# Kernel tuning notes

Hardware: AMD Instinct MI355X
Metric: run time of the kernel (lower is better)

Reference implementation:

```python
import jax, jax.numpy as jnp
import numpy as np

BETA = 0.25
K = 1024   # num_codebook_vectors
D = 256    # latent_dim


def setup_inputs() -> dict:
    key = jax.random.key(0)
    k1, k2 = jax.random.split(key)
    z = jax.random.normal(k1, (16, D, 64, 64), dtype=jnp.float32)
    # embedding initialized uniform(-1/K, 1/K) as in the torch module
    emb = jax.random.uniform(k2, (K, D), dtype=jnp.float32, minval=-1.0 / K, maxval=1.0 / K)
    return {"z": z, "emb": emb}


def reference(z, emb):
    sg = jax.lax.stop_gradient
    # NCHW -> NHWC
    z_nhwc = jnp.transpose(z, (0, 2, 3, 1))            # [B,H,W,D]
    zf = z_nhwc.reshape(-1, D)                          # [N,D]
    # squared euclidean distances: ||z||^2 + ||e||^2 - 2 z e^T
    d = (jnp.sum(zf * zf, axis=1, keepdims=True)
         + jnp.sum(emb * emb, axis=1)
         - 2.0 * jnp.matmul(zf, emb.T))                 # [N,K]
    min_encoding_indices = jnp.argmin(d, axis=1)        # [N] int
    z_q = emb[min_encoding_indices].reshape(z_nhwc.shape)  # [B,H,W,D]
    # loss exactly as in source (first term is zero in value, faithful)
    loss = (jnp.mean((sg(z_nhwc) - z_nhwc) ** 2)
            + BETA * jnp.mean((z_q - sg(z_nhwc)) ** 2))
    # straight-through estimator
    z_q_st = z_nhwc + sg(z_q - z_nhwc)
    out = jnp.transpose(z_q_st, (0, 3, 1, 2))           # NHWC -> NCHW
    return out, min_encoding_indices, loss
```

## Files before the change

kernel.cpp:

```cpp
#include <hip/hip_runtime.h>

#define DD 256
#define KK 1024
#define HW 4096
#define NROWSZ 65536
#define OUT_Z 16777216
#define OUT_IDX OUT_Z
#define OUT_LOSS (OUT_Z + NROWSZ)

#define MARGIN 4.5e-4f

#define WS_ESQ   0
#define WS_EH    4096
#define WS_HLIST 528384
#define WS_HCNT  790528
#define WS_LSUM  790536
#define WS_EMBT  791552
#define WS_EHP   1840128

typedef _Float16 f16x8 __attribute__((ext_vector_type(8)));
typedef float f32x4 __attribute__((ext_vector_type(4)));
union U16x8 { uint4 u; f16x8 h; };
typedef unsigned long long u64;

static __device__ __forceinline__ u64 umin64(u64 a, u64 b) { return a < b ? a : b; }
static __device__ __forceinline__ unsigned pk16(float a, float b) {
    _Float16 ha = (_Float16)a, hb = (_Float16)b;
    return (unsigned)__builtin_bit_cast(unsigned short, ha)
         | ((unsigned)__builtin_bit_cast(unsigned short, hb) << 16);
}

__global__ void vq_prep(const float* __restrict__ emb, float* __restrict__ esq,
                        uint2* __restrict__ eh2, int* __restrict__ hcnt,
                        double* __restrict__ lsum, float* __restrict__ embT,
                        int use_embT, uint4* __restrict__ ehP, int use_ehp)
{
    const int bid = blockIdx.x;
    const int t = threadIdx.x;
    if (bid == 0 && t == 0) { *hcnt = 0; *lsum = 0.0; }

    if (bid < 4) {
        int k = bid * 256 + t;
        const float* e = emb + (size_t)k * DD;
        float blk[2];
#pragma unroll
        for (int b2 = 0; b2 < 2; ++b2) {
            const float* p = e + b2 * 128;
            float r[8];
#pragma unroll
            for (int j = 0; j < 8; ++j) r[j] = __fmul_rn(p[j], p[j]);
            for (int i = 8; i < 128; i += 8) {
#pragma unroll
                for (int j = 0; j < 8; ++j)
                    r[j] = __fadd_rn(r[j], __fmul_rn(p[i + j], p[i + j]));
            }
            blk[b2] = __fadd_rn(__fadd_rn(__fadd_rn(r[0], r[1]), __fadd_rn(r[2], r[3])),
                                __fadd_rn(__fadd_rn(r[4], r[5]), __fadd_rn(r[6], r[7])));
        }
        esq[k] = __fadd_rn(blk[0], blk[1]);
    } else if (bid < 20) {
        int tid = (bid - 4) * 256 + t;
        const float4* e4 = (const float4*)emb;
#pragma unroll
        for (int i = 0; i < 16; ++i) {
            int idx = i * 4096 + tid;
            float4 v = e4[idx];
            eh2[idx] = make_uint2(pk16(v.x, v.y), pk16(v.z, v.w));
        }
    } else if (bid < 36) {
        if (!use_embT) return;
        int u = bid - 20;
        int k = u * 64 + (t >> 2);
        int c = t & 3;
        const float4* e4 = (const float4*)(emb + (size_t)k * DD);
#pragma unroll
        for (int i = 0; i < 16; ++i) {
            float4 v = e4[c * 16 + i];
            int d = c * 64 + i * 4;
            embT[(size_t)(d + 0) * KK + k] = v.x;
            embT[(size_t)(d + 1) * KK + k] = v.y;
            embT[(size_t)(d + 2) * KK + k] = v.z;
            embT[(size_t)(d + 3) * KK + k] = v.w;
        }
    } else {
        if (!use_ehp) return;
#pragma unroll
        for (int it = 0; it < 8; ++it) {
            int L = ((bid - 36) * 8 + it) * 256 + t;
            int lane = L & 63, ds = (L >> 6) & 7, t16 = L >> 9;
            int col = lane & 15, quad = lane >> 4;
            int code = t16 * 16 + col;
            int d0 = ds * 32 + quad * 8;
            const float* e = emb + (size_t)code * DD + d0;
            float4 a = *(const float4*)e;
            float4 c4 = *(const float4*)(e + 4);
            ehP[L] = make_uint4(pk16(a.x, a.y), pk16(a.z, a.w),
                                pk16(c4.x, c4.y), pk16(c4.z, c4.w));
        }
    }
}

__launch_bounds__(512, 2)
__global__ void vq_score(const float* __restrict__ z, const _Float16* __restrict__ eh,
                         const uint4* __restrict__ ehP, const float* __restrict__ esq,
                         float* __restrict__ out, int* __restrict__ hlist,
                         int* __restrict__ hcnt, int use_ehp)
{
    __shared__ __align__(16) char zh[256 * 512];
    __shared__ float esq_s[1024];
    __shared__ uint2 cand[256];

    const int t = threadIdx.x;
    const int lane = t & 63;
    const int w = t >> 6;
    const int col = lane & 15;
    const int quad = lane >> 4;

    const int n0 = blockIdx.x * 256;
    const int b = n0 >> 12;
    const int hw0 = n0 & (HW - 1);

    {
        const int row = t & 255;
        const int dh = t >> 8;
        const float* src = z + (size_t)b * DD * HW + hw0 + row;
#pragma unroll
        for (int i = 0; i < 16; ++i) {
            const int d0 = dh * 128 + i * 8;
            float v0 = src[(size_t)(d0 + 0) * HW];
            float v1 = src[(size_t)(d0 + 1) * HW];
            float v2 = src[(size_t)(d0 + 2) * HW];
            float v3 = src[(size_t)(d0 + 3) * HW];
            float v4 = src[(size_t)(d0 + 4) * HW];
            float v5 = src[(size_t)(d0 + 5) * HW];
            float v6 = src[(size_t)(d0 + 6) * HW];
            float v7 = src[(size_t)(d0 + 7) * HW];
            uint4 pk = make_uint4(pk16(v0, v1), pk16(v2, v3), pk16(v4, v5), pk16(v6, v7));
            *(uint4*)(zh + (size_t)row * 512 + ((d0 * 2) ^ ((row & 7) << 4))) = pk;
        }
        esq_s[t] = esq[t];
        esq_s[512 + t] = esq[512 + t];
    }
    __syncthreads();

    U16x8 af[2][8];
#pragma unroll
    for (int nt = 0; nt < 2; ++nt) {
        const int row = w * 32 + nt * 16 + col;
        const int sw = (row & 7) << 4;
#pragma unroll
        for (int ds = 0; ds < 8; ++ds)
            af[nt][ds].u = *(const uint4*)(zh + (size_t)row * 512
                                           + ((ds * 64 + quad * 16) ^ sw));
    }

    unsigned t1[8], t2[8];
#pragma unroll
    for (int i = 0; i < 8; ++i) { t1[i] = 0xFFFFFFFFu; t2[i] = 0xFFFFFFFFu; }

    auto proc = [&](U16x8 (&bf)[8], int t16) {
        const int code = t16 * 16 + col;
        const float eq1 = 1.0f + esq_s[code];
        f32x4 acc0 = (f32x4)0.0f, acc1 = (f32x4)0.0f;
#pragma unroll
        for (int ds = 0; ds < 8; ++ds) {
            acc0 = __builtin_amdgcn_mfma_f32_16x16x32_f16(af[0][ds].h, bf[ds].h, acc0, 0, 0, 0);
            acc1 = __builtin_amdgcn_mfma_f32_16x16x32_f16(af[1][ds].h, bf[ds].h, acc1, 0, 0, 0);
        }
#pragma unroll
        for (int r = 0; r < 4; ++r) {
            float s0 = fmaf(-2.0f, acc0[r], eq1);
            unsigned k0 = (__float_as_uint(s0) & 0xFFFFFC00u) | (unsigned)code;
            t2[r] = min(t2[r], max(t1[r], k0));
            t1[r] = min(t1[r], k0);
            float s1 = fmaf(-2.0f, acc1[r], eq1);
            unsigned k1 = (__float_as_uint(s1) & 0xFFFFFC00u) | (unsigned)code;
            t2[4 + r] = min(t2[4 + r], max(t1[4 + r], k1));
            t1[4 + r] = min(t1[4 + r], k1);
        }
    };

    if (use_ehp) {
        const uint4* bq = ehP + lane;
        U16x8 bfA[8], bfB[8];
#pragma unroll
        for (int ds = 0; ds < 8; ++ds) bfA[ds].u = bq[ds * 64];
#pragma unroll 1
        for (int t16 = 0; t16 < 64; t16 += 2) {
            const uint4* p1 = bq + (size_t)(t16 + 1) * 512;
#pragma unroll
            for (int ds = 0; ds < 8; ++ds) bfB[ds].u = p1[ds * 64];
            proc(bfA, t16);
            const uint4* p2 = bq + (size_t)((t16 + 2) & 63) * 512;
#pragma unroll
            for (int ds = 0; ds < 8; ++ds) bfA[ds].u = p2[ds * 64];
            proc(bfB, t16 + 1);
            if ((t16 & 6) == 6) __builtin_amdgcn_s_barrier();
        }
    } else {
        const uint4* ehq = (const uint4*)eh;
#pragma unroll 1
        for (int t16 = 0; t16 < 64; ++t16) {
            const uint4* bp = ehq + (size_t)(t16 * 16 + col) * 32 + quad;
            U16x8 bf[8];
#pragma unroll
            for (int ds = 0; ds < 8; ++ds) bf[ds].u = bp[ds * 4];
            proc(bf, t16);
        }
    }

#pragma unroll
    for (int mi = 0; mi < 8; ++mi) {
        unsigned a = t1[mi], bb = t2[mi];
#pragma unroll
        for (int off = 1; off < 16; off <<= 1) {
            unsigned o1 = __shfl_xor(a, off, 16);
            unsigned o2 = __shfl_xor(bb, off, 16);
            unsigned mx = max(a, o1);
            a = min(a, o1);
            bb = min(min(bb, o2), mx);
        }
        if (col == 0)
            cand[w * 32 + (mi >> 2) * 16 + quad * 4 + (mi & 3)] = make_uint2(a, bb);
    }
    __syncthreads();

    if (t < 256) {
        uint2 c = cand[t];
        float s1 = __uint_as_float(c.x & 0xFFFFFC00u);
        float s2 = __uint_as_float(c.y & 0xFFFFFC00u);
        int k1 = (int)(c.x & 1023u);
        if (__fsub_rn(s2, s1) > MARGIN) {
            out[OUT_IDX + n0 + t] = (float)k1;
        } else {
            int pos = atomicAdd(hcnt, 1);
            hlist[pos] = n0 + t;
        }
    }
}

template<int USET>
static __device__ __forceinline__ void dot_codes(const float4* __restrict__ embT4,
                                                 const float4* __restrict__ emb4,
                                                 const float4* __restrict__ zb4,
                                                 int t, float (&acc_)[8][4])
{
#pragma unroll 2
    for (int dc = 0; dc < 64; ++dc) {
        float4 e0, e1, e2, e3;
        if (USET) {
            e0 = embT4[(size_t)(dc * 4 + 0) * 256 + t];
            e1 = embT4[(size_t)(dc * 4 + 1) * 256 + t];
            e2 = embT4[(size_t)(dc * 4 + 2) * 256 + t];
            e3 = embT4[(size_t)(dc * 4 + 3) * 256 + t];
        } else {
            float4 a0 = emb4[(size_t)(4 * t + 0) * 64 + dc];
            float4 a1 = emb4[(size_t)(4 * t + 1) * 64 + dc];
            float4 a2 = emb4[(size_t)(4 * t + 2) * 64 + dc];
            float4 a3 = emb4[(size_t)(4 * t + 3) * 64 + dc];
            e0 = make_float4(a0.x, a1.x, a2.x, a3.x);
            e1 = make_float4(a0.y, a1.y, a2.y, a3.y);
            e2 = make_float4(a0.z, a1.z, a2.z, a3.z);
            e3 = make_float4(a0.w, a1.w, a2.w, a3.w);
        }
#pragma unroll
        for (int j = 0; j < 8; ++j) {
            float4 zv = zb4[j * 64 + dc];
            acc_[j][0] = fmaf(zv.x, e0.x, acc_[j][0]);
            acc_[j][1] = fmaf(zv.x, e0.y, acc_[j][1]);
            acc_[j][2] = fmaf(zv.x, e0.z, acc_[j][2]);
            acc_[j][3] = fmaf(zv.x, e0.w, acc_[j][3]);
            acc_[j][0] = fmaf(zv.y, e1.x, acc_[j][0]);
            acc_[j][1] = fmaf(zv.y, e1.y, acc_[j][1]);
            acc_[j][2] = fmaf(zv.y, e1.z, acc_[j][2]);
            acc_[j][3] = fmaf(zv.y, e1.w, acc_[j][3]);
            acc_[j][0] = fmaf(zv.z, e2.x, acc_[j][0]);
            acc_[j][1] = fmaf(zv.z, e2.y, acc_[j][1]);
            acc_[j][2] = fmaf(zv.z, e2.z, acc_[j][2]);
            acc_[j][3] = fmaf(zv.z, e2.w, acc_[j][3]);
            acc_[j][0] = fmaf(zv.w, e3.x, acc_[j][0]);
            acc_[j][1] = fmaf(zv.w, e3.y, acc_[j][1]);
            acc_[j][2] = fmaf(zv.w, e3.z, acc_[j][2]);
            acc_[j][3] = fmaf(zv.w, e3.w, acc_[j][3]);
        }
    }
}

__launch_bounds__(256)
__global__ void vq_hard(const float* __restrict__ z, const float* __restrict__ emb,
                        const float* __restrict__ embT, const float* __restrict__ esq,
                        const int* __restrict__ hlist, const int* __restrict__ hcnt,
                        float* __restrict__ out, int use_embT)
{
    __shared__ __align__(16) float zbuf[8 * 256];
    __shared__ float chains[8][16];
    __shared__ float zq_s[8];
    __shared__ int rows_s[8];
    __shared__ u64 red[4][8];

    const int t = threadIdx.x;
    const int lane = t & 63;
    const int w = t >> 6;
    const int count = *hcnt;

    const float4* embT4 = (const float4*)embT;
    const float4* emb4 = (const float4*)emb;
    const float4* zb4 = (const float4*)zbuf;
    const float4 eqv4 = ((const float4*)esq)[t];
    const float eqa[4] = {eqv4.x, eqv4.y, eqv4.z, eqv4.w};

    for (int g = blockIdx.x; g * 8 < count; g += gridDim.x) {
        __syncthreads();
        if (t < 8) {
            int p = g * 8 + t;
            rows_s[t] = (p < count) ? hlist[p] : -1;
        }
        __syncthreads();

        {
            const int j = t >> 5, dpos = t & 31;
            const int r = rows_s[j];
            float4 v0 = make_float4(0.f, 0.f, 0.f, 0.f), v1 = v0;
            if (r >= 0) {
                const float* zp = z + (size_t)(r >> 12) * (DD * HW) + (r & (HW - 1));
                const int d0 = dpos * 8;
                v0.x = zp[(size_t)(d0 + 0) * HW];
                v0.y = zp[(size_t)(d0 + 1) * HW];
                v0.z = zp[(size_t)(d0 + 2) * HW];
                v0.w = zp[(size_t)(d0 + 3) * HW];
                v1.x = zp[(size_t)(d0 + 4) * HW];
                v1.y = zp[(size_t)(d0 + 5) * HW];
                v1.z = zp[(size_t)(d0 + 6) * HW];
                v1.w = zp[(size_t)(d0 + 7) * HW];
            }
            *(float4*)&zbuf[j * 256 + dpos * 8] = v0;
            *(float4*)&zbuf[j * 256 + dpos * 8 + 4] = v1;
        }
        __syncthreads();

        if (t < 128) {
            int j = t >> 4, c = t & 15, b2 = c >> 3, jj = c & 7;
            const float* p = &zbuf[j * 256];
            int base = b2 * 128 + jj;
            float v = p[base];
            float acc = __fmul_rn(v, v);
            for (int i = 1; i < 16; ++i) {
                float u = p[base + i * 8];
                acc = __fadd_rn(acc, __fmul_rn(u, u));
            }
            chains[j][c] = acc;
        }
        __syncthreads();
        if (t < 8) {
            const float* c = chains[t];
            float b0 = __fadd_rn(__fadd_rn(__fadd_rn(c[0], c[1]), __fadd_rn(c[2], c[3])),
                                 __fadd_rn(__fadd_rn(c[4], c[5]), __fadd_rn(c[6], c[7])));
            float b1 = __fadd_rn(__fadd_rn(__fadd_rn(c[8], c[9]), __fadd_rn(c[10], c[11])),
                                 __fadd_rn(__fadd_rn(c[12], c[13]), __fadd_rn(c[14], c[15])));
            zq_s[t] = __fadd_rn(b0, b1);
        }
        __syncthreads();

        float acc_[8][4];
#pragma unroll
        for (int j = 0; j < 8; ++j)
#pragma unroll
            for (int kk = 0; kk < 4; ++kk) acc_[j][kk] = 0.0f;

        if (use_embT) dot_codes<1>(embT4, emb4, zb4, t, acc_);
        else          dot_codes<0>(embT4, emb4, zb4, t, acc_);

#pragma unroll
        for (int j = 0; j < 8; ++j) {
            u64 m = ~0ull;
#pragma unroll
            for (int kk = 0; kk < 4; ++kk) {
                float s = __fsub_rn(__fadd_rn(zq_s[j], eqa[kk]),
                                    __fmul_rn(2.0f, acc_[j][kk]));
                u64 p = ((u64)__float_as_uint(s) << 32) | (unsigned)(4 * t + kk);
                m = umin64(m, p);
            }
#pragma unroll
            for (int off = 1; off < 64; off <<= 1)
                m = umin64(m, __shfl_xor(m, off, 64));
            if (lane == 0) red[w][j] = m;
        }
        __syncthreads();
        if (t < 8) {
            u64 m = umin64(umin64(red[0][t], red[1][t]), umin64(red[2][t], red[3][t]));
            int r = rows_s[t];
            if (r >= 0) out[OUT_IDX + r] = (float)(int)(m & 0xffffffffu);
        }
    }
}

__launch_bounds__(256)
__global__ void vq_out(const float* __restrict__ z, const float* __restrict__ emb,
                       const float* __restrict__ embT, float* out,
                       double* __restrict__ lsum, int use_embT)
{
    __shared__ float et[8 * 1024];
    __shared__ float wsum[4];

    const int t = threadIdx.x;
    const int lane = t & 63;
    const int w = t >> 6;
    const int bb = blockIdx.x >> 5;
    const int dg = blockIdx.x & 31;

    if (use_embT) {
#pragma unroll
        for (int c = 0; c < 8; ++c)
            *(float4*)&et[c * 1024 + t * 4] =
                *(const float4*)&embT[(size_t)(dg * 8 + c) * KK + t * 4];
    } else {
        for (int i = 0; i < 32; ++i) {
            int kk = i * 256 + t;
            et[kk] = emb[(size_t)(kk & 1023) * DD + dg * 8 + (kk >> 10)];
        }
    }
    __syncthreads();

    float lacc = 0.f;
    const size_t zb = (size_t)bb * DD * HW;
    const float* idxf = out + OUT_IDX + (size_t)bb * HW;
#pragma unroll
    for (int ch = 0; ch < 4; ++ch) {
        const int hw = ch * 1024 + t * 4;
        float4 fi = *(const float4*)&idxf[hw];
        int k0 = (int)fi.x, k1 = (int)fi.y, k2 = (int)fi.z, k3 = (int)fi.w;
#pragma unroll
        for (int dl = 0; dl < 8; ++dl) {
            size_t off = zb + (size_t)(dg * 8 + dl) * HW + hw;
            float4 zv = *(const float4*)&z[off];
            float4 e;
            e.x = et[dl * 1024 + k0];
            e.y = et[dl * 1024 + k1];
            e.z = et[dl * 1024 + k2];
            e.w = et[dl * 1024 + k3];
            *(float4*)&out[off] = e;
            float df;
            df = e.x - zv.x; lacc = fmaf(df, df, lacc);
            df = e.y - zv.y; lacc = fmaf(df, df, lacc);
            df = e.z - zv.z; lacc = fmaf(df, df, lacc);
            df = e.w - zv.w; lacc = fmaf(df, df, lacc);
        }
    }
#pragma unroll
    for (int off = 32; off > 0; off >>= 1) lacc += __shfl_down(lacc, off, 64);
    if (lane == 0) wsum[w] = lacc;
    __syncthreads();
    if (t == 0) {
        double tot = (double)wsum[0] + (double)wsum[1] + (double)wsum[2] + (double)wsum[3];
        atomicAdd(lsum, tot);
    }
}

__global__ void vq_final(const double* __restrict__ lsum, float* __restrict__ out)
{
    out[OUT_LOSS] = (float)(0.25 * (lsum[0] / (double)OUT_Z));
}

extern "C" void kernel_launch(void* const* d_in, const int* in_sizes, int n_in,
                              void* d_out, int out_size, void* d_ws, size_t ws_size,
                              hipStream_t stream)
{
    const float* z = (const float*)d_in[0];
    const float* emb = (const float*)d_in[1];
    float* out = (float*)d_out;
    char* w = (char*)d_ws;

    float* esq = (float*)(w + WS_ESQ);
    _Float16* eh = (_Float16*)(w + WS_EH);
    uint2* eh2 = (uint2*)(w + WS_EH);
    int* hlist = (int*)(w + WS_HLIST);
    int* hcnt = (int*)(w + WS_HCNT);
    double* lsum = (double*)(w + WS_LSUM);
    float* embT = (float*)(w + WS_EMBT);
    uint4* ehP = (uint4*)(w + WS_EHP);

    int use_embT = (ws_size >= (size_t)WS_EMBT + (size_t)DD * KK * sizeof(float)) ? 1 : 0;
    int use_ehp = (ws_size >= (size_t)WS_EHP + (size_t)KK * DD * sizeof(_Float16)) ? 1 : 0;

    vq_prep<<<dim3(52), dim3(256), 0, stream>>>(emb, esq, eh2, hcnt, lsum, embT, use_embT,
                                                ehP, use_ehp);
    vq_score<<<dim3(256), dim3(512), 0, stream>>>(z, eh, ehP, esq, out, hlist, hcnt,
                                                  use_ehp);
    vq_hard<<<dim3(1024), dim3(256), 0, stream>>>(z, emb, embT, esq, hlist, hcnt, out,
                                                  use_embT);
    vq_out<<<dim3(512), dim3(256), 0, stream>>>(z, emb, embT, out, lsum, use_embT);
    vq_final<<<dim3(1), dim3(1), 0, stream>>>(lsum, out);
}
```

Baseline: 247.4 us.

## Shrink vq_score and vq_out tiles to launch more blocks across CUs

vq_score now handles 64 rows per 256-thread block instead of 256 rows per 512-thread block. Each wave computes one 16-row MFMA tile instead of two, and the double-buffered codebook prefetch and periodic barrier are dropped. vq_out now covers 4 latent channels per block instead of 8, which doubles its grid. The aim is to fill all 256 CUs of the MI355X with more, smaller blocks. The cost is that each codebook fragment loaded from global memory now feeds only one MFMA tile, and without software prefetch there is less latency hiding.

```diff
diff --git a/kernel.cpp b/kernel.cpp
--- a/kernel.cpp
+++ b/kernel.cpp
@@ -100,15 +100,15 @@
     }
 }
 
-__launch_bounds__(512, 2)
+__launch_bounds__(256, 4)
 __global__ void vq_score(const float* __restrict__ z, const _Float16* __restrict__ eh,
                          const uint4* __restrict__ ehP, const float* __restrict__ esq,
                          float* __restrict__ out, int* __restrict__ hlist,
                          int* __restrict__ hcnt, int use_ehp)
 {
-    __shared__ __align__(16) char zh[256 * 512];
+    __shared__ __align__(16) char zh[64 * 512];
     __shared__ float esq_s[1024];
-    __shared__ uint2 cand[256];
+    __shared__ uint2 cand[64];
 
     const int t = threadIdx.x;
     const int lane = t & 63;
@@ -116,17 +116,15 @@
     const int col = lane & 15;
     const int quad = lane >> 4;
 
-    const int n0 = blockIdx.x * 256;
+    const int n0 = blockIdx.x * 64;
     const int b = n0 >> 12;
     const int hw0 = n0 & (HW - 1);
 
     {
-        const int row = t & 255;
-        const int dh = t >> 8;
-        const float* src = z + (size_t)b * DD * HW + hw0 + row;
-#pragma unroll
-        for (int i = 0; i < 16; ++i) {
-            const int d0 = dh * 128 + i * 8;
+        const float* src = z + (size_t)b * DD * HW + hw0 + lane;
+#pragma unroll
+        for (int i = 0; i < 8; ++i) {
+            const int d0 = w * 64 + i * 8;
             float v0 = src[(size_t)(d0 + 0) * HW];
             float v1 = src[(size_t)(d0 + 1) * HW];
             float v2 = src[(size_t)(d0 + 2) * HW];
@@ -136,81 +134,77 @@
             float v6 = src[(size_t)(d0 + 6) * HW];
             float v7 = src[(size_t)(d0 + 7) * HW];
             uint4 pk = make_uint4(pk16(v0, v1), pk16(v2, v3), pk16(v4, v5), pk16(v6, v7));
-            *(uint4*)(zh + (size_t)row * 512 + ((d0 * 2) ^ ((row & 7) << 4))) = pk;
+            *(uint4*)(zh + (size_t)lane * 512 + ((d0 * 2) ^ ((lane & 7) << 4))) = pk;
         }
         esq_s[t] = esq[t];
+        esq_s[256 + t] = esq[256 + t];
         esq_s[512 + t] = esq[512 + t];
+        esq_s[768 + t] = esq[768 + t];
     }
     __syncthreads();
 
-    U16x8 af[2][8];
-#pragma unroll
-    for (int nt = 0; nt < 2; ++nt) {
-        const int row = w * 32 + nt * 16 + col;
-        const int sw = (row & 7) << 4;
+    U16x8 af[8];
+    {
+        const int arow = w * 16 + col;
+        const int sw = (arow & 7) << 4;
 #pragma unroll
         for (int ds = 0; ds < 8; ++ds)
-            af[nt][ds].u = *(const uint4*)(zh + (size_t)row * 512
-                                           + ((ds * 64 + quad * 16) ^ sw));
-    }
-
-    unsigned t1[8], t2[8];
-#pragma unroll
-    for (int i = 0; i < 8; ++i) { t1[i] = 0xFFFFFFFFu; t2[i] = 0xFFFFFFFFu; }
-
-    auto proc = [&](U16x8 (&bf)[8], int t16) {
-        const int code = t16 * 16 + col;
-        const float eq1 = 1.0f + esq_s[code];
-        f32x4 acc0 = (f32x4)0.0f, acc1 = (f32x4)0.0f;
-#pragma unroll
-        for (int ds = 0; ds < 8; ++ds) {
-            acc0 = __builtin_amdgcn_mfma_f32_16x16x32_f16(af[0][ds].h, bf[ds].h, acc0, 0, 0, 0);
-            acc1 = __builtin_amdgcn_mfma_f32_16x16x32_f16(af[1][ds].h, bf[ds].h, acc1, 0, 0, 0);
-        }
-#pragma unroll
-        for (int r = 0; r < 4; ++r) {
-            float s0 = fmaf(-2.0f, acc0[r], eq1);
-            unsigned k0 = (__float_as_uint(s0) & 0xFFFFFC00u) | (unsigned)code;
-            t2[r] = min(t2[r], max(t1[r], k0));
-            t1[r] = min(t1[r], k0);
-            float s1 = fmaf(-2.0f, acc1[r], eq1);
-            unsigned k1 = (__float_as_uint(s1) & 0xFFFFFC00u) | (unsigned)code;
-            t2[4 + r] = min(t2[4 + r], max(t1[4 + r], k1));
-            t1[4 + r] = min(t1[4 + r], k1);
-        }
-    };
+            af[ds].u = *(const uint4*)(zh + (size_t)arow * 512
+                                       + ((ds * 64 + quad * 16) ^ sw));
+    }
+
+    unsigned t1[4], t2[4];
+#pragma unroll
+    for (int i = 0; i < 4; ++i) { t1[i] = 0xFFFFFFFFu; t2[i] = 0xFFFFFFFFu; }
 
     if (use_ehp) {
         const uint4* bq = ehP + lane;
-        U16x8 bfA[8], bfB[8];
-#pragma unroll
-        for (int ds = 0; ds < 8; ++ds) bfA[ds].u = bq[ds * 64];
 #pragma unroll 1
-        for (int t16 = 0; t16 < 64; t16 += 2) {
-            const uint4* p1 = bq + (size_t)(t16 + 1) * 512;
-#pragma unroll
-            for (int ds = 0; ds < 8; ++ds) bfB[ds].u = p1[ds * 64];
-            proc(bfA, t16);
-            const uint4* p2 = bq + (size_t)((t16 + 2) & 63) * 512;
-#pragma unroll
-            for (int ds = 0; ds < 8; ++ds) bfA[ds].u = p2[ds * 64];
-            proc(bfB, t16 + 1);
-            if ((t16 & 6) == 6) __builtin_amdgcn_s_barrier();
+        for (int t16 = 0; t16 < 64; ++t16) {
+            const uint4* p = bq + (size_t)t16 * 512;
+            U16x8 bf[8];
+#pragma unroll
+            for (int ds = 0; ds < 8; ++ds) bf[ds].u = p[ds * 64];
+            const int code = t16 * 16 + col;
+            const float eq1 = 1.0f + esq_s[code];
+            f32x4 acc = (f32x4)0.0f;
+#pragma unroll
+            for (int ds = 0; ds < 8; ++ds)
+                acc = __builtin_amdgcn_mfma_f32_16x16x32_f16(af[ds].h, bf[ds].h, acc, 0, 0, 0);
+#pragma unroll
+            for (int r = 0; r < 4; ++r) {
+                float s = fmaf(-2.0f, acc[r], eq1);
+                unsigned k = (__float_as_uint(s) & 0xFFFFFC00u) | (unsigned)code;
+                t2[r] = min(t2[r], max(t1[r], k));
+                t1[r] = min(t1[r], k);
+            }
         }
     } else {
         const uint4* ehq = (const uint4*)eh;
 #pragma unroll 1
         for (int t16 = 0; t16 < 64; ++t16) {
-            const uint4* bp = ehq + (size_t)(t16 * 16 + col) * 32 + quad;
+            const int code = t16 * 16 + col;
+            const uint4* bp = ehq + (size_t)code * 32 + quad;
             U16x8 bf[8];
 #pragma unroll
             for (int ds = 0; ds < 8; ++ds) bf[ds].u = bp[ds * 4];
-            proc(bf, t16);
-        }
-    }
-
-#pragma unroll
-    for (int mi = 0; mi < 8; ++mi) {
+            const float eq1 = 1.0f + esq_s[code];
+            f32x4 acc = (f32x4)0.0f;
+#pragma unroll
+            for (int ds = 0; ds < 8; ++ds)
+                acc = __builtin_amdgcn_mfma_f32_16x16x32_f16(af[ds].h, bf[ds].h, acc, 0, 0, 0);
+#pragma unroll
+            for (int r = 0; r < 4; ++r) {
+                float s = fmaf(-2.0f, acc[r], eq1);
+                unsigned k = (__float_as_uint(s) & 0xFFFFFC00u) | (unsigned)code;
+                t2[r] = min(t2[r], max(t1[r], k));
+                t1[r] = min(t1[r], k);
+            }
+        }
+    }
+
+#pragma unroll
+    for (int mi = 0; mi < 4; ++mi) {
         unsigned a = t1[mi], bb = t2[mi];
 #pragma unroll
         for (int off = 1; off < 16; off <<= 1) {
@@ -221,11 +215,11 @@
             bb = min(min(bb, o2), mx);
         }
         if (col == 0)
-            cand[w * 32 + (mi >> 2) * 16 + quad * 4 + (mi & 3)] = make_uint2(a, bb);
+            cand[w * 16 + quad * 4 + mi] = make_uint2(a, bb);
     }
     __syncthreads();
 
-    if (t < 256) {
+    if (t < 64) {
         uint2 c = cand[t];
         float s1 = __uint_as_float(c.x & 0xFFFFFC00u);
         float s2 = __uint_as_float(c.y & 0xFFFFFC00u);
@@ -399,24 +393,24 @@
                        const float* __restrict__ embT, float* out,
                        double* __restrict__ lsum, int use_embT)
 {
-    __shared__ float et[8 * 1024];
+    __shared__ float et[4 * 1024];
     __shared__ float wsum[4];
 
     const int t = threadIdx.x;
     const int lane = t & 63;
     const int w = t >> 6;
-    const int bb = blockIdx.x >> 5;
-    const int dg = blockIdx.x & 31;
+    const int bb = blockIdx.x >> 6;
+    const int dg = blockIdx.x & 63;
 
     if (use_embT) {
 #pragma unroll
-        for (int c = 0; c < 8; ++c)
+        for (int c = 0; c < 4; ++c)
             *(float4*)&et[c * 1024 + t * 4] =
-                *(const float4*)&embT[(size_t)(dg * 8 + c) * KK + t * 4];
+                *(const float4*)&embT[(size_t)(dg * 4 + c) * KK + t * 4];
     } else {
-        for (int i = 0; i < 32; ++i) {
+        for (int i = 0; i < 16; ++i) {
             int kk = i * 256 + t;
-            et[kk] = emb[(size_t)(kk & 1023) * DD + dg * 8 + (kk >> 10)];
+            et[kk] = emb[(size_t)(kk & 1023) * DD + dg * 4 + (kk >> 10)];
         }
     }
     __syncthreads();
@@ -430,8 +424,8 @@
         float4 fi = *(const float4*)&idxf[hw];
         int k0 = (int)fi.x, k1 = (int)fi.y, k2 = (int)fi.z, k3 = (int)fi.w;
 #pragma unroll
-        for (int dl = 0; dl < 8; ++dl) {
-            size_t off = zb + (size_t)(dg * 8 + dl) * HW + hw;
+        for (int dl = 0; dl < 4; ++dl) {
+            size_t off = zb + (size_t)(dg * 4 + dl) * HW + hw;
             float4 zv = *(const float4*)&z[off];
             float4 e;
             e.x = et[dl * 1024 + k0];
@@ -484,10 +478,10 @@
 
     vq_prep<<<dim3(52), dim3(256), 0, stream>>>(emb, esq, eh2, hcnt, lsum, embT, use_embT,
                                                 ehP, use_ehp);
-    vq_score<<<dim3(256), dim3(512), 0, stream>>>(z, eh, ehP, esq, out, hlist, hcnt,
-                                                  use_ehp);
+    vq_score<<<dim3(1024), dim3(256), 0, stream>>>(z, eh, ehP, esq, out, hlist, hcnt,
+                                                   use_ehp);
     vq_hard<<<dim3(1024), dim3(256), 0, stream>>>(z, emb, embT, esq, hlist, hcnt, out,
                                                   use_embT);
-    vq_out<<<dim3(512), dim3(256), 0, stream>>>(z, emb, embT, out, lsum, use_embT);
+    vq_out<<<dim3(1024), dim3(256), 0, stream>>>(z, emb, embT, out, lsum, use_embT);
     vq_final<<<dim3(1), dim3(1), 0, stream>>>(lsum, out);
 }
```

Result: slower. 265.4 us (+7.3%).

## Halve per-block work in score and output kernels to double grid size

Applied to the files above, without the earlier changes.

The scoring kernel now handles 128 rows per 256-thread block instead of 256 rows per 512-thread block. It stages z through a smaller 64-row shared buffer in two passes, so LDS use drops from 128KB to 32KB and more blocks can be resident. The output kernel processes 4 channels per block instead of 8 and launches twice as many blocks. The aim is better occupancy and more blocks across the CUs, at the cost of extra barriers and duplicated esq and embedding loads per block.

```diff
diff --git a/kernel.cpp b/kernel.cpp
--- a/kernel.cpp
+++ b/kernel.cpp
@@ -100,15 +100,15 @@
     }
 }
 
-__launch_bounds__(512, 2)
+__launch_bounds__(256, 2)
 __global__ void vq_score(const float* __restrict__ z, const _Float16* __restrict__ eh,
                          const uint4* __restrict__ ehP, const float* __restrict__ esq,
                          float* __restrict__ out, int* __restrict__ hlist,
                          int* __restrict__ hcnt, int use_ehp)
 {
-    __shared__ __align__(16) char zh[256 * 512];
+    __shared__ __align__(16) char zh[64 * 512];
     __shared__ float esq_s[1024];
-    __shared__ uint2 cand[256];
+    __shared__ uint2 cand[128];
 
     const int t = threadIdx.x;
     const int lane = t & 63;
@@ -116,42 +116,54 @@
     const int col = lane & 15;
     const int quad = lane >> 4;
 
-    const int n0 = blockIdx.x * 256;
+    const int n0 = blockIdx.x * 128;
     const int b = n0 >> 12;
     const int hw0 = n0 & (HW - 1);
 
+    esq_s[t] = esq[t];
+    esq_s[256 + t] = esq[256 + t];
+    esq_s[512 + t] = esq[512 + t];
+    esq_s[768 + t] = esq[768 + t];
+
+    U16x8 af[2][8];
     {
-        const int row = t & 255;
-        const int dh = t >> 8;
-        const float* src = z + (size_t)b * DD * HW + hw0 + row;
-#pragma unroll
-        for (int i = 0; i < 16; ++i) {
-            const int d0 = dh * 128 + i * 8;
-            float v0 = src[(size_t)(d0 + 0) * HW];
-            float v1 = src[(size_t)(d0 + 1) * HW];
-            float v2 = src[(size_t)(d0 + 2) * HW];
-            float v3 = src[(size_t)(d0 + 3) * HW];
-            float v4 = src[(size_t)(d0 + 4) * HW];
-            float v5 = src[(size_t)(d0 + 5) * HW];
-            float v6 = src[(size_t)(d0 + 6) * HW];
-            float v7 = src[(size_t)(d0 + 7) * HW];
-            uint4 pk = make_uint4(pk16(v0, v1), pk16(v2, v3), pk16(v4, v5), pk16(v6, v7));
-            *(uint4*)(zh + (size_t)row * 512 + ((d0 * 2) ^ ((row & 7) << 4))) = pk;
-        }
-        esq_s[t] = esq[t];
-        esq_s[512 + t] = esq[512 + t];
-    }
-    __syncthreads();
-
-    U16x8 af[2][8];
-#pragma unroll
-    for (int nt = 0; nt < 2; ++nt) {
-        const int row = w * 32 + nt * 16 + col;
-        const int sw = (row & 7) << 4;
-#pragma unroll
-        for (int ds = 0; ds < 8; ++ds)
-            af[nt][ds].u = *(const uint4*)(zh + (size_t)row * 512
-                                           + ((ds * 64 + quad * 16) ^ sw));
+        const int rl = t & 63, dg = t >> 6;
+#pragma unroll
+        for (int c = 0; c < 2; ++c) {
+            const float* src = z + (size_t)b * DD * HW + hw0 + c * 64 + rl;
+#pragma unroll
+            for (int i = 0; i < 2; ++i) {
+                const int d0 = dg * 64 + i * 32;
+#pragma unroll
+                for (int j = 0; j < 4; ++j) {
+                    const int dd = d0 + j * 8;
+                    float v0 = src[(size_t)(dd + 0) * HW];
+                    float v1 = src[(size_t)(dd + 1) * HW];
+                    float v2 = src[(size_t)(dd + 2) * HW];
+                    float v3 = src[(size_t)(dd + 3) * HW];
+                    float v4 = src[(size_t)(dd + 4) * HW];
+                    float v5 = src[(size_t)(dd + 5) * HW];
+                    float v6 = src[(size_t)(dd + 6) * HW];
+                    float v7 = src[(size_t)(dd + 7) * HW];
+                    uint4 pk = make_uint4(pk16(v0, v1), pk16(v2, v3),
+                                          pk16(v4, v5), pk16(v6, v7));
+                    *(uint4*)(zh + (size_t)rl * 512 + ((dd * 2) ^ ((rl & 7) << 4))) = pk;
+                }
+            }
+            __syncthreads();
+            if ((w >> 1) == c) {
+#pragma unroll
+                for (int nt = 0; nt < 2; ++nt) {
+                    const int lr = (w & 1) * 32 + nt * 16 + col;
+                    const int sw = (lr & 7) << 4;
+#pragma unroll
+                    for (int ds = 0; ds < 8; ++ds)
+                        af[nt][ds].u = *(const uint4*)(zh + (size_t)lr * 512
+                                                       + ((ds * 64 + quad * 16) ^ sw));
+                }
+            }
+            __syncthreads();
+        }
     }
 
     unsigned t1[8], t2[8];
@@ -225,7 +237,7 @@
     }
     __syncthreads();
 
-    if (t < 256) {
+    if (t < 128) {
         uint2 c = cand[t];
         float s1 = __uint_as_float(c.x & 0xFFFFFC00u);
         float s2 = __uint_as_float(c.y & 0xFFFFFC00u);
@@ -399,24 +411,24 @@
                        const float* __restrict__ embT, float* out,
                        double* __restrict__ lsum, int use_embT)
 {
-    __shared__ float et[8 * 1024];
+    __shared__ float et[4 * 1024];
     __shared__ float wsum[4];
 
     const int t = threadIdx.x;
     const int lane = t & 63;
     const int w = t >> 6;
-    const int bb = blockIdx.x >> 5;
-    const int dg = blockIdx.x & 31;
+    const int bb = blockIdx.x >> 6;
+    const int dg = blockIdx.x & 63;
 
     if (use_embT) {
 #pragma unroll
-        for (int c = 0; c < 8; ++c)
+        for (int c = 0; c < 4; ++c)
             *(float4*)&et[c * 1024 + t * 4] =
-                *(const float4*)&embT[(size_t)(dg * 8 + c) * KK + t * 4];
+                *(const float4*)&embT[(size_t)(dg * 4 + c) * KK + t * 4];
     } else {
-        for (int i = 0; i < 32; ++i) {
+        for (int i = 0; i < 16; ++i) {
             int kk = i * 256 + t;
-            et[kk] = emb[(size_t)(kk & 1023) * DD + dg * 8 + (kk >> 10)];
+            et[kk] = emb[(size_t)(kk & 1023) * DD + dg * 4 + (kk >> 10)];
         }
     }
     __syncthreads();
@@ -430,8 +442,8 @@
         float4 fi = *(const float4*)&idxf[hw];
         int k0 = (int)fi.x, k1 = (int)fi.y, k2 = (int)fi.z, k3 = (int)fi.w;
 #pragma unroll
-        for (int dl = 0; dl < 8; ++dl) {
-            size_t off = zb + (size_t)(dg * 8 + dl) * HW + hw;
+        for (int dl = 0; dl < 4; ++dl) {
+            size_t off = zb + (size_t)(dg * 4 + dl) * HW + hw;
             float4 zv = *(const float4*)&z[off];
             float4 e;
             e.x = et[dl * 1024 + k0];
@@ -484,10 +496,10 @@
 
     vq_prep<<<dim3(52), dim3(256), 0, stream>>>(emb, esq, eh2, hcnt, lsum, embT, use_embT,
                                                 ehP, use_ehp);
-    vq_score<<<dim3(256), dim3(512), 0, stream>>>(z, eh, ehP, esq, out, hlist, hcnt,
+    vq_score<<<dim3(512), dim3(256), 0, stream>>>(z, eh, ehP, esq, out, hlist, hcnt,
                                                   use_ehp);
     vq_hard<<<dim3(1024), dim3(256), 0, stream>>>(z, emb, embT, esq, hlist, hcnt, out,
                                                   use_embT);
-    vq_out<<<dim3(512), dim3(256), 0, stream>>>(z, emb, embT, out, lsum, use_embT);
+    vq_out<<<dim3(1024), dim3(256), 0, stream>>>(z, emb, embT, out, lsum, use_embT);
     vq_final<<<dim3(1), dim3(1), 0, stream>>>(lsum, out);
 }
```

Measured after the change: 252.2 us. No clear change (+1.9%).
